# Kernel optimization log

Measured on AMD Instinct MI355X. Metric: run time of the kernel, lower is better.

Reference implementation:

```python
import jax, jax.numpy as jnp
import numpy as np

UNITS = 256
B, T_IN, F_IN = 1024, 128, 3
OUT_STEPS = 32


def setup_inputs() -> dict:
    key = jax.random.key(0)
    ks = jax.random.split(key, 6)
    inputs = jax.random.normal(ks[0], (B, T_IN, F_IN), dtype=jnp.float32)
    Wk = jax.random.normal(ks[1], (F_IN, 4 * UNITS), dtype=jnp.float32) * 0.1
    Wr = jax.random.normal(ks[2], (UNITS, 4 * UNITS), dtype=jnp.float32) * 0.1
    b = jax.random.normal(ks[3], (4 * UNITS,), dtype=jnp.float32) * 0.1
    Wd = jax.random.normal(ks[4], (UNITS, 3), dtype=jnp.float32) * 0.1
    bd = jax.random.normal(ks[5], (3,), dtype=jnp.float32) * 0.1
    return {"inputs": inputs, "Wk": Wk, "Wr": Wr, "b": b,
            "Wd": Wd, "bd": bd, "out_steps": OUT_STEPS}


def _lstm_cell(x, h, c, Wk, Wr, b):
    # Keras LSTMCell: gates ordered i, f, g(candidate), o
    z = x @ Wk + h @ Wr + b                      # [B, 4U]
    i, f, g, o = jnp.split(z, 4, axis=-1)
    i = jax.nn.sigmoid(i)
    f = jax.nn.sigmoid(f)
    o = jax.nn.sigmoid(o)
    c_new = f * c + i * jnp.tanh(g)
    h_new = o * jnp.tanh(c_new)
    return h_new, c_new


def reference(inputs, Wk, Wr, b, Wd, bd, out_steps):
    Bsz = inputs.shape[0]
    units = Wr.shape[0]
    h0 = jnp.zeros((Bsz, units), dtype=inputs.dtype)
    c0 = jnp.zeros((Bsz, units), dtype=inputs.dtype)

    # --- warmup: run LSTM over the input sequence, keep final state ---
    def warm_step(carry, x_t):
        h, c = carry
        h, c = _lstm_cell(x_t, h, c, Wk, Wr, b)
        return (h, c), None

    xs = jnp.transpose(inputs, (1, 0, 2))        # [T, B, F]
    (h, c), _ = jax.lax.scan(warm_step, (h0, c0), xs)

    pred0 = h @ Wd + bd                          # [B, 3]

    if out_steps == 1:
        return pred0[:, None, :]

    def dec_step(carry, _):
        h, c, pred = carry
        h, c = _lstm_cell(pred, h, c, Wk, Wr, b)
        new_pred = h @ Wd + bd
        return (h, c, new_pred), new_pred

    _, preds_rest = jax.lax.scan(dec_step, (h, c, pred0), None,
                                 length=out_steps - 1)   # [S-1, B, 3]
    preds = jnp.concatenate([pred0[None], preds_rest], axis=0)  # [S, B, 3]
    return jnp.transpose(preds, (1, 0, 2))       # [B, S, 3]
```

## Files before the change

kernel.cpp:

```cpp
#include <hip/hip_runtime.h>


#define TIN    128
#define FIN    3
#define OSTEPS 32
#define LASTT  (TIN + OSTEPS - 1)

typedef float    f32x4 __attribute__((ext_vector_type(4)));
typedef _Float16 half8 __attribute__((ext_vector_type(8)));
typedef unsigned long long u64;

__device__ __forceinline__ float fast_rcp(float x) { return __builtin_amdgcn_rcpf(x); }
__device__ __forceinline__ float sigm(float x)  { return fast_rcp(1.0f + __expf(-x)); }
__device__ __forceinline__ float tanh_f(float x){ return 1.0f - 2.0f * fast_rcp(__expf(2.0f * x) + 1.0f); }

__global__ __launch_bounds__(512) void pack_wr(const float* __restrict__ Wr,
                                               _Float16* __restrict__ P)
{
    int idx = blockIdx.x * 512 + threadIdx.x;
    int l   = idx & 63;
    int kt  = (idx >> 6) & 7;
    int T   = idx >> 9;
    int p = T >> 5, q = (T >> 3) & 3, w = T & 7;
    int col = q * 256 + p * 128 + w * 16 + (l & 15);
    int k0  = kt * 32 + (l >> 4) * 8;
    half8 v;
#pragma unroll
    for (int j = 0; j < 8; ++j) v[j] = (_Float16)Wr[(k0 + j) * 1024 + col];
    *reinterpret_cast<half8*>(P + (size_t)idx * 8) = v;
}

__global__ __launch_bounds__(512, 2) void lstm_pair(
    const float* __restrict__ x_in,
    const float* __restrict__ Wk,
    const float* __restrict__ bias,
    const float* __restrict__ Wd,
    const float* __restrict__ bd,
    const _Float16* __restrict__ WrP,
    u64*       __restrict__ hex,
    unsigned*  __restrict__ flags,
    float* __restrict__ out)
{
    __shared__ float                xs[16 * TIN * FIN];
    __shared__ alignas(16) _Float16 hfull[2][4096];
    __shared__ float                pred_buf[16][4];

    const int tid  = threadIdx.x;
    const int w    = tid >> 6;
    const int l    = tid & 63;
    const int n    = l & 15;
    const int row0 = (l >> 4) * 4;
    const int bid  = blockIdx.x;
    const int p    = (bid >> 3) & 1;
    const int pp   = 1 - p;
    const int g    = (bid & 7) + 8 * (bid >> 4);

    const float* xsrc = x_in + (size_t)g * 16 * TIN * FIN;
    for (int i = tid; i < 16 * TIN * FIN; i += 512) xs[i] = xsrc[i];

    half8 bfr[4][8];
#pragma unroll
    for (int q = 0; q < 4; ++q)
#pragma unroll
        for (int kt = 0; kt < 8; ++kt)
            bfr[q][kt] = *reinterpret_cast<const half8*>(
                WrP + (((size_t)(p * 32 + q * 8 + w) * 8 + kt) * 512 + l * 8));

    float b_r[4], wk_r[4][3];
#pragma unroll
    for (int q = 0; q < 4; ++q) {
        int col = q * 256 + p * 128 + w * 16 + n;
        b_r[q] = bias[col];
#pragma unroll
        for (int f = 0; f < 3; ++f) wk_r[q][f] = Wk[f * 1024 + col];
    }
    float wd_r[4][3];
#pragma unroll
    for (int j = 0; j < 4; ++j)
#pragma unroll
        for (int f = 0; f < 3; ++f) wd_r[j][f] = Wd[(4 * l + j) * 3 + f];
    const float bd0 = bd[0], bd1 = bd[1], bd2 = bd[2];

    float c_st[4] = {0.f, 0.f, 0.f, 0.f};
    const int hpos = p * 2048 + (w >> 1) * 512 + ((2 * w + (n >> 3)) & 3) * 128
                   + row0 * 8 + (n & 7);

    unsigned* cnt_my   = flags + ((size_t)g * 2 + p)  * 16;
    unsigned* cnt_peer = flags + ((size_t)g * 2 + pp) * 16;

    __syncthreads();

    for (int t = 0; t <= LASTT; ++t) {
        const int par_rd = (t - 1) & 1;

        if (t > 0) {
            if (tid == 0) {
                while (__hip_atomic_load(cnt_peer, __ATOMIC_RELAXED,
                                         __HIP_MEMORY_SCOPE_AGENT) < (unsigned)t) { }
            }
            __syncthreads();
            const u64* hexr = hex + ((size_t)(par_rd * 64 + g)) * 1024 + pp * 512;
            u64 v = __hip_atomic_load(hexr + tid, __ATOMIC_RELAXED,
                                      __HIP_MEMORY_SCOPE_AGENT);
            reinterpret_cast<u64*>(&hfull[par_rd][pp * 2048])[tid] = v;
            __syncthreads();
        }

        if (t >= TIN) {
            const int s = t - TIN;
#pragma unroll
            for (int rr = 0; rr < 2; ++rr) {
                int row = 2 * w + rr;
                const _Float16* hb = &hfull[par_rd][(l >> 3) * 512
                                   + ((l >> 1) & 3) * 128 + row * 8 + 4 * (l & 1)];
                float p0 = 0.f, p1 = 0.f, p2 = 0.f;
#pragma unroll
                for (int j = 0; j < 4; ++j) {
                    float hj = (float)hb[j];
                    p0 += hj * wd_r[j][0];
                    p1 += hj * wd_r[j][1];
                    p2 += hj * wd_r[j][2];
                }
#pragma unroll
                for (int o = 32; o > 0; o >>= 1) {
                    p0 += __shfl_xor(p0, o);
                    p1 += __shfl_xor(p1, o);
                    p2 += __shfl_xor(p2, o);
                }
                if (l == 0) {
                    p0 += bd0; p1 += bd1; p2 += bd2;
                    pred_buf[row][0] = p0; pred_buf[row][1] = p1; pred_buf[row][2] = p2;
                    if (p == 0) {
                        float* op = out + ((size_t)(g * 16 + row) * OSTEPS + s) * 3;
                        op[0] = p0; op[1] = p1; op[2] = p2;
                    }
                }
            }
            __syncthreads();
            if (t == LASTT) break;
        }

        half8 a[8];
        if (t > 0) {
#pragma unroll
            for (int kt = 0; kt < 8; ++kt)
                a[kt] = *reinterpret_cast<const half8*>(&hfull[par_rd][kt * 512 + l * 8]);
        } else {
            half8 az = {};
#pragma unroll
            for (int kt = 0; kt < 8; ++kt) a[kt] = az;
        }

        float xv[4][3];
#pragma unroll
        for (int r = 0; r < 4; ++r) {
            int row = row0 + r;
            if (t >= TIN) {
                xv[r][0] = pred_buf[row][0];
                xv[r][1] = pred_buf[row][1];
                xv[r][2] = pred_buf[row][2];
            } else {
                const float* xp = &xs[(row * TIN + t) * 3];
                xv[r][0] = xp[0]; xv[r][1] = xp[1]; xv[r][2] = xp[2];
            }
        }

        f32x4 acc[4];
#pragma unroll
        for (int q = 0; q < 4; ++q)
#pragma unroll
            for (int r = 0; r < 4; ++r)
                acc[q][r] = b_r[q] + xv[r][0] * wk_r[q][0]
                          + xv[r][1] * wk_r[q][1] + xv[r][2] * wk_r[q][2];
#pragma unroll
        for (int kt = 0; kt < 8; ++kt)
#pragma unroll
            for (int q = 0; q < 4; ++q)
                acc[q] = __builtin_amdgcn_mfma_f32_16x16x32_f16(a[kt], bfr[q][kt], acc[q], 0, 0, 0);

        const int par_wr = t & 1;
#pragma unroll
        for (int r = 0; r < 4; ++r) {
            float iv = sigm(acc[0][r]);
            float fv = sigm(acc[1][r]);
            float gv = tanh_f(acc[2][r]);
            float ov = sigm(acc[3][r]);
            float cc = fv * c_st[r] + iv * gv;
            c_st[r] = cc;
            hfull[par_wr][hpos + r * 8] = (_Float16)(ov * tanh_f(cc));
        }
        __syncthreads();

        {
            u64 v = reinterpret_cast<const u64*>(&hfull[par_wr][p * 2048])[tid];
            u64* hexw = hex + ((size_t)(par_wr * 64 + g)) * 1024 + p * 512;
            __hip_atomic_store(hexw + tid, v, __ATOMIC_RELAXED,
                               __HIP_MEMORY_SCOPE_AGENT);
        }
        __syncthreads();
        if (tid == 0)
            __hip_atomic_store(cnt_my, (unsigned)(t + 1), __ATOMIC_RELAXED,
                               __HIP_MEMORY_SCOPE_AGENT);
    }
}

extern "C" void kernel_launch(void* const* d_in, const int* in_sizes, int n_in,
                              void* d_out, int out_size, void* d_ws, size_t ws_size,
                              hipStream_t stream)
{
    const float* x  = (const float*)d_in[0];
    const float* Wk = (const float*)d_in[1];
    const float* Wr = (const float*)d_in[2];
    const float* b  = (const float*)d_in[3];
    const float* Wd = (const float*)d_in[4];
    const float* bd = (const float*)d_in[5];
    float* out = (float*)d_out;

    unsigned* flags = (unsigned*)d_ws;
    _Float16* WrP   = (_Float16*)((char*)d_ws + 8192);
    u64*      hex   = (u64*)((char*)d_ws + 8192 + 524288);

    hipMemsetAsync(d_ws, 0, 8192, stream);
    pack_wr<<<64, 512, 0, stream>>>(Wr, WrP);
    lstm_pair<<<128, 512, 0, stream>>>(x, Wk, b, Wd, bd, WrP, hex, flags, out);
}
```

Measured before the change: 427.4 us.

## Replace counter-flag handoff with per-element tagged hidden-state exchange

Each hidden value is published to global memory as a 32-bit word carrying its fp16 value plus the timestep tag. The peer block spins on the words themselves until every tag matches. This removes the separate flag store and flag poll, plus two block barriers per step, shortening the cross-block handoff on the critical recurrence path. In exchange it doubles exchange traffic, adds per-thread spinning on global loads, and adds a larger memset to initialise the tags.

```diff
diff --git a/kernel.cpp b/kernel.cpp
--- a/kernel.cpp
+++ b/kernel.cpp
@@ -9,6 +9,7 @@
 typedef float    f32x4 __attribute__((ext_vector_type(4)));
 typedef _Float16 half8 __attribute__((ext_vector_type(8)));
 typedef unsigned long long u64;
+typedef unsigned int u32;
 
 __device__ __forceinline__ float fast_rcp(float x) { return __builtin_amdgcn_rcpf(x); }
 __device__ __forceinline__ float sigm(float x)  { return fast_rcp(1.0f + __expf(-x)); }
@@ -37,8 +38,7 @@
     const float* __restrict__ Wd,
     const float* __restrict__ bd,
     const _Float16* __restrict__ WrP,
-    u64*       __restrict__ hex,
-    unsigned*  __restrict__ flags,
+    u32*   __restrict__ hexT,
     float* __restrict__ out)
 {
     __shared__ float                xs[16 * TIN * FIN];
@@ -82,11 +82,9 @@
     const float bd0 = bd[0], bd1 = bd[1], bd2 = bd[2];
 
     float c_st[4] = {0.f, 0.f, 0.f, 0.f};
-    const int hpos = p * 2048 + (w >> 1) * 512 + ((2 * w + (n >> 3)) & 3) * 128
+    const int hloc = (w >> 1) * 512 + ((2 * w + (n >> 3)) & 3) * 128
                    + row0 * 8 + (n & 7);
-
-    unsigned* cnt_my   = flags + ((size_t)g * 2 + p)  * 16;
-    unsigned* cnt_peer = flags + ((size_t)g * 2 + pp) * 16;
+    const int hpos = p * 2048 + hloc;
 
     __syncthreads();
 
@@ -94,15 +92,22 @@
         const int par_rd = (t - 1) & 1;
 
         if (t > 0) {
-            if (tid == 0) {
-                while (__hip_atomic_load(cnt_peer, __ATOMIC_RELAXED,
-                                         __HIP_MEMORY_SCOPE_AGENT) < (unsigned)t) { }
-            }
-            __syncthreads();
-            const u64* hexr = hex + ((size_t)(par_rd * 64 + g)) * 1024 + pp * 512;
-            u64 v = __hip_atomic_load(hexr + tid, __ATOMIC_RELAXED,
-                                      __HIP_MEMORY_SCOPE_AGENT);
-            reinterpret_cast<u64*>(&hfull[par_rd][pp * 2048])[tid] = v;
+            const u64* src = reinterpret_cast<const u64*>(
+                hexT + (((size_t)par_rd * 64 + g) * 2 + pp) * 2048) + tid * 2;
+            const u64 msk = 0x0000FFFF0000FFFFull;
+            const u64 tg2 = (u64)(u32)(t - 1) * 0x0000000100000001ull;
+            u64 w0, w1;
+            do {
+                w0 = __hip_atomic_load(src + 0, __ATOMIC_RELAXED,
+                                       __HIP_MEMORY_SCOPE_AGENT);
+                w1 = __hip_atomic_load(src + 1, __ATOMIC_RELAXED,
+                                       __HIP_MEMORY_SCOPE_AGENT);
+            } while (((w0 & msk) != tg2) || ((w1 & msk) != tg2));
+            u64 hv = ((w0 >> 16) & 0xFFFFull)
+                   | ((w0 >> 48) << 16)
+                   | (((w1 >> 16) & 0xFFFFull) << 32)
+                   | ((w1 >> 48) << 48);
+            reinterpret_cast<u64*>(&hfull[par_rd][pp * 2048])[tid] = hv;
             __syncthreads();
         }
 
@@ -179,6 +184,7 @@
                 acc[q] = __builtin_amdgcn_mfma_f32_16x16x32_f16(a[kt], bfr[q][kt], acc[q], 0, 0, 0);
 
         const int par_wr = t & 1;
+        u32* wdst = hexT + (((size_t)par_wr * 64 + g) * 2 + p) * 2048 + hloc;
 #pragma unroll
         for (int r = 0; r < 4; ++r) {
             float iv = sigm(acc[0][r]);
@@ -187,20 +193,12 @@
             float ov = sigm(acc[3][r]);
             float cc = fv * c_st[r] + iv * gv;
             c_st[r] = cc;
-            hfull[par_wr][hpos + r * 8] = (_Float16)(ov * tanh_f(cc));
-        }
-        __syncthreads();
-
-        {
-            u64 v = reinterpret_cast<const u64*>(&hfull[par_wr][p * 2048])[tid];
-            u64* hexw = hex + ((size_t)(par_wr * 64 + g)) * 1024 + p * 512;
-            __hip_atomic_store(hexw + tid, v, __ATOMIC_RELAXED,
+            _Float16 hh = (_Float16)(ov * tanh_f(cc));
+            hfull[par_wr][hpos + r * 8] = hh;
+            u32 tw = ((u32)__builtin_bit_cast(unsigned short, hh) << 16) | (u32)t;
+            __hip_atomic_store(wdst + r * 8, tw, __ATOMIC_RELAXED,
                                __HIP_MEMORY_SCOPE_AGENT);
         }
-        __syncthreads();
-        if (tid == 0)
-            __hip_atomic_store(cnt_my, (unsigned)(t + 1), __ATOMIC_RELAXED,
-                               __HIP_MEMORY_SCOPE_AGENT);
     }
 }
 
@@ -216,11 +214,10 @@
     const float* bd = (const float*)d_in[5];
     float* out = (float*)d_out;
 
-    unsigned* flags = (unsigned*)d_ws;
-    _Float16* WrP   = (_Float16*)((char*)d_ws + 8192);
-    u64*      hex   = (u64*)((char*)d_ws + 8192 + 524288);
-
-    hipMemsetAsync(d_ws, 0, 8192, stream);
+    _Float16* WrP  = (_Float16*)d_ws;
+    u32*      hexT = (u32*)((char*)d_ws + 524288);
+
+    hipMemsetAsync(hexT, 0xFF, 2097152, stream);
     pack_wr<<<64, 512, 0, stream>>>(Wr, WrP);
-    lstm_pair<<<128, 512, 0, stream>>>(x, Wk, b, Wd, bd, WrP, hex, flags, out);
+    lstm_pair<<<128, 512, 0, stream>>>(x, Wk, b, Wd, bd, WrP, hexT, out);
 }
```

After: 627.4 us. 1.47x slower.
